# Kernel tuning notes

Measured on AMD Instinct MI355X. Metric: run time of the kernel, lower is better.

## Reference

```python
import jax, jax.numpy as jnp
import numpy as np

BS, T, D_IN = 128, 32, 128
DH = 128          # controller hidden size == memory word width M
N_SLOTS = 512     # memory rows
EPS = 1e-8


def _split_read(o):
    # o: [bs, M+6] -> k, beta, g, s(3), gamma
    k = o[:, :DH]
    beta = jax.nn.softplus(o[:, DH])
    g = jax.nn.sigmoid(o[:, DH + 1])
    s = jax.nn.softmax(o[:, DH + 2:DH + 5], axis=-1)
    gamma = 1.0 + jax.nn.softplus(o[:, DH + 5])
    return k, beta, g, s, gamma


def _attention(k, beta, g, s, gamma, mem, w_prev):
    # content addressing: cosine similarity sharpened by beta
    dot = jnp.einsum('bnm,bm->bn', mem, k)
    denom = jnp.linalg.norm(mem, axis=-1) * jnp.linalg.norm(k, axis=-1, keepdims=True) + EPS
    w_c = jax.nn.softmax(beta[:, None] * dot / denom, axis=-1)
    # gate interpolation with previous weights
    w_g = g[:, None] * w_c + (1.0 - g[:, None]) * w_prev
    # circular shift convolution over offsets {-1, 0, +1}
    w_t = (s[:, 0:1] * jnp.roll(w_g, -1, axis=-1)
           + s[:, 1:2] * w_g
           + s[:, 2:3] * jnp.roll(w_g, 1, axis=-1))
    # sharpening
    w = w_t ** gamma[:, None]
    return w / (jnp.sum(w, axis=-1, keepdims=True) + EPS)


def setup_inputs() -> dict:
    key = jax.random.key(0)
    ks = jax.random.split(key, 8)
    sc = lambda fan_in: 1.0 / np.sqrt(fan_in)
    return {
        'x':    jax.random.normal(ks[0], (BS, T, D_IN), jnp.float32),
        'Wxh':  jax.random.normal(ks[1], (D_IN, DH), jnp.float32) * sc(D_IN),
        'Whh':  jax.random.normal(ks[2], (DH, DH), jnp.float32) * sc(DH),
        'Wrh':  jax.random.normal(ks[3], (DH, DH), jnp.float32) * sc(DH),
        'bh':   jnp.zeros((DH,), jnp.float32),
        'Wout': jax.random.normal(ks[4], (DH + DH, D_IN), jnp.float32) * sc(2 * DH),
        'bout': jnp.zeros((D_IN,), jnp.float32),
        'Wr':   jax.random.normal(ks[5], (DH, DH + 6), jnp.float32) * sc(DH),
        'br':   jnp.zeros((DH + 6,), jnp.float32),
        'Ww':   jax.random.normal(ks[6], (DH, 3 * DH + 6), jnp.float32) * sc(DH),
        'bw':   jnp.zeros((3 * DH + 6,), jnp.float32),
    }


def reference(x, Wxh, Whh, Wrh, bh, Wout, bout, Wr, br, Ww, bw):
    bs = x.shape[0]
    h0 = jnp.zeros((bs, DH), x.dtype)
    r0 = jnp.zeros((bs, DH), x.dtype)
    w0 = jnp.full((bs, N_SLOTS), 1.0 / N_SLOTS, x.dtype)
    mem0 = jnp.full((bs, N_SLOTS, DH), 1e-6, x.dtype)

    def step(carry, x_t):
        h, r, w_prev, mem = carry
        # controller state
        h = jnp.tanh(x_t @ Wxh + h @ Whh + r @ Wrh + bh)
        # head parameter projections
        o_r = h @ Wr + br
        o_w = h @ Ww + bw
        k_r, b_r, g_r, s_r, y_r = _split_read(o_r)
        k_w, b_w_, g_w, s_w, y_w = _split_read(o_w[:, :DH + 6])
        e = jax.nn.sigmoid(o_w[:, DH + 6:2 * DH + 6])   # erase [bs, M]
        a = jnp.tanh(o_w[:, 2 * DH + 6:3 * DH + 6])     # add   [bs, M]
        # addressing (w_previous updated sequentially, read then write)
        w_r = _attention(k_r, b_r, g_r, s_r, y_r, mem, w_prev)
        w_w = _attention(k_w, b_w_, g_w, s_w, y_w, mem, w_r)
        # read
        r = jnp.einsum('bn,bnm->bm', w_r, mem)
        # erase / add write
        mem = mem * (1.0 - w_w[:, :, None] * e[:, None, :]) + w_w[:, :, None] * a[:, None, :]
        # output
        y = jnp.concatenate([h, r], axis=-1) @ Wout + bout
        return (h, r, w_w, mem), y

    _, ys = jax.lax.scan(step, (h0, r0, w0, mem0), jnp.swapaxes(x, 0, 1))
    return jnp.swapaxes(ys, 0, 1)  # [bs, ft, d_output]
```

## Files before the change

### kernel.cpp

```cpp
#include <hip/hip_runtime.h>
#include <hip/hip_bf16.h>
#include <math.h>

#define NT 1024
#define BSZ 128
#define TSTEPS 32
#define DIN 128
#define DHH 128
#define NSLOT 512
#define EPSF 1e-8f

static constexpr int F_FLOATS = 7160;
static constexpr size_t LDS_BYTES = 131072 + F_FLOATS * sizeof(float);

__device__ __forceinline__ float bf_lo(unsigned u) {
  union { unsigned u; float f; } c; c.u = u << 16; return c.f;
}
__device__ __forceinline__ float bf_hi(unsigned u) {
  union { unsigned u; float f; } c; c.u = u & 0xffff0000u; return c.f;
}
__device__ __forceinline__ unsigned short f2us(float f) {
  union { unsigned short s; __hip_bfloat16 h; } c; c.h = __float2bfloat16(f); return c.s;
}
__device__ __forceinline__ unsigned pkbf(float a, float b) {
  union { __hip_bfloat162 h2; unsigned u; } c;
  c.h2 = __float22bfloat162_rn(make_float2(a, b));
  return c.u;
}
__device__ __forceinline__ float sigmoid_(float x) { return 1.0f / (1.0f + __expf(-x)); }
__device__ __forceinline__ float softplus_(float x) {
  return fmaxf(x, 0.0f) + log1pf(__expf(-fabsf(x)));
}
__device__ __forceinline__ float tanh_(float x) {
  float e = __expf(-2.0f * fabsf(x));
  float t = (1.0f - e) / (1.0f + e);
  return copysignf(t, x);
}
__device__ __forceinline__ float waveSum(float v) {
#pragma unroll
  for (int m = 32; m >= 1; m >>= 1) v += __shfl_xor(v, m);
  return v;
}

__device__ __forceinline__ void bar_lds() {
  asm volatile("s_waitcnt lgkmcnt(0)" ::: "memory");
  __builtin_amdgcn_s_barrier();
}

__global__ __launch_bounds__(NT, 4)
void ntm_kernel(const float* __restrict__ x,
                const float* __restrict__ Wxh,
                const float* __restrict__ Whh,
                const float* __restrict__ Wrh,
                const float* __restrict__ bh,
                const float* __restrict__ Wout,
                const float* __restrict__ bout,
                const float* __restrict__ Wr,
                const float* __restrict__ br,
                const float* __restrict__ Ww,
                const float* __restrict__ bw,
                float* __restrict__ out)
{
  extern __shared__ char smem[];
  uint4* memv = (uint4*)smem;
  float* F = (float*)(smem + 131072);

  const int b = blockIdx.x;
  const int tid = threadIdx.x;
  const int g = tid >> 4, l = tid & 15;
  const int lane = tid & 63, wid = tid >> 6;

  float* U      = F + 0;
  float* yP     = F + 2560;
  float* sWprev = F + 4608;
  float* sP1    = F + 5632;
  float* sOr    = F + 6144;
  float* sOw    = F + 6288;
  float* sXt    = F + 6680;
  float* sH     = F + 6808;
  float* sR     = F + 6936;
  float* sP     = F + 7064;
  float* V      = sXt;
  uint4* krP    = (uint4*)(sP1 + 0);
  uint4* kwP    = (uint4*)(sP1 + 64);
  float* eR     = U + 0;
  float* eW     = U + 512;
  float2* sWW2  = (float2*)(U + 1024);

  {
    const unsigned short mb = f2us(1e-6f);
    const unsigned w32 = ((unsigned)mb << 16) | mb;
    const uint4 fv = make_uint4(w32, w32, w32, w32);
    for (int i = tid; i < NSLOT * DHH / 8; i += NT) memv[i] = fv;
  }
  for (int i = tid; i < NSLOT; i += NT) sWprev[i] = 1.0f / NSLOT;
  if (tid < DHH) { sH[tid] = 0.0f; sR[tid] = 0.0f; }
  if (tid < DIN) sXt[tid] = x[(size_t)b * TSTEPS * DIN + tid];
  __syncthreads();

  for (int t = 0; t < TSTEPS; ++t) {
    {
      const int q = tid & 63, s = tid >> 6;
      const int j2 = q * 2, i0 = s * 24;
      float2 acc = make_float2(0.f, 0.f);
#pragma unroll 2
      for (int k = 0; k < 6; ++k) {
        const float4 vv = *(const float4*)(V + i0 + 4 * k);
        const float vk[4] = { vv.x, vv.y, vv.z, vv.w };
#pragma unroll
        for (int u = 0; u < 4; ++u) {
          const int i = i0 + 4 * k + u;
          const float* Wp = (i < 128) ? (Wxh + i * DHH)
                          : (i < 256) ? (Whh + (i - 128) * DHH)
                                      : (Wrh + (i - 256) * DHH);
          const float2 wv = *(const float2*)(Wp + j2);
          acc.x = fmaf(vk[u], wv.x, acc.x);
          acc.y = fmaf(vk[u], wv.y, acc.y);
        }
      }
      *(float2*)(U + s * 128 + j2) = acc;
      if (t > 0 && tid < 512) {
        const int j4 = (tid & 31) * 4, sl = tid >> 5;
        float4 acc4 = *(const float4*)(yP + sl * 128 + j4);
#pragma unroll
        for (int w = 0; w < 8; ++w) {
          const float v = sR[8 * sl + w];
          const float4 wv = *(const float4*)(Wout + (128 + 8 * sl + w) * DIN + j4);
          acc4.x = fmaf(v, wv.x, acc4.x); acc4.y = fmaf(v, wv.y, acc4.y);
          acc4.z = fmaf(v, wv.z, acc4.z); acc4.w = fmaf(v, wv.w, acc4.w);
        }
        *(float4*)(yP + sl * 128 + j4) = acc4;
      }
      bar_lds();
    }
    if (tid < DHH) {
      float a2 = bh[tid];
#pragma unroll
      for (int q2 = 0; q2 < 16; ++q2) a2 += U[q2 * 128 + tid];
      sH[tid] = tanh_(a2);
    }
    bar_lds();

    {
      {
        const int s = tid;
        const int q = (s >= 786) ? 3 : (s >= 524) ? 2 : (s >= 262) ? 1 : 0;
        const int P = s - 262 * q;
        const int i0 = 32 * q;
        const float2* p;
        int strideF2;
        if (P < 67) { p = (const float2*)(Wr + i0 * 134 + 2 * P); strideF2 = 67; }
        else        { p = (const float2*)(Ww + i0 * 390 + 2 * (P - 67)); strideF2 = 195; }
        float2 acc = make_float2(0.f, 0.f);
#pragma unroll 2
        for (int k = 0; k < 8; ++k) {
          const float4 hv = *(const float4*)(sH + i0 + 4 * k);
          const float hk[4] = { hv.x, hv.y, hv.z, hv.w };
#pragma unroll
          for (int u = 0; u < 4; ++u) {
            const float2 wv = p[(4 * k + u) * strideF2];
            acc.x = fmaf(hk[u], wv.x, acc.x);
            acc.y = fmaf(hk[u], wv.y, acc.y);
          }
        }
        *(float2*)(U + s * 2) = acc;
      }
      if (lane < 3) {
        const int hs = wid * 3 + lane;
        const int e = hs >> 1, hh = hs & 1;
        const int cp = 171 + e;
        const int i0 = 96 + 16 * hh;
        const float2* p = (const float2*)(Ww + i0 * 390 + 2 * cp);
        float2 acc = make_float2(0.f, 0.f);
#pragma unroll 8
        for (int w = 0; w < 16; ++w) {
          const float v = sH[i0 + w];
          const float2 wv = *p;
          acc.x = fmaf(v, wv.x, acc.x);
          acc.y = fmaf(v, wv.y, acc.y);
          p += 195;
        }
        U[2096 + hs * 2]     = acc.x;
        U[2096 + hs * 2 + 1] = acc.y;
      }
      if (tid == 1023) {
        sP[0] = 0.f; sP[1] = 0.f; sP[2] = 0.f; sP[3] = 0.f; sP[4] = 0.f; sP[5] = 0.f;
      }
      bar_lds();
    }

    {
      if (tid < 134) {
        float v = 0.f;
#pragma unroll
        for (int q = 0; q < 4; ++q) v += U[tid + 524 * q];
        v += br[tid];
        sOr[tid] = v;
        if (tid < 128) {
          float s2 = waveSum(v * v);
          if (lane == 0) atomicAdd(&sP[0], s2);
        }
      } else if (tid == 134) {
        float sc[6];
#pragma unroll
        for (int j = 0; j < 6; ++j) {
          float v = 0.f;
#pragma unroll
          for (int q = 0; q < 4; ++q) v += U[(128 + j) + 524 * q];
          sc[j] = v + br[128 + j];
        }
        sP[80] = softplus_(sc[0]);
        sP[81] = sigmoid_(sc[1]);
        float mx = fmaxf(sc[2], fmaxf(sc[3], sc[4]));
        float e0 = __expf(sc[2] - mx), e1 = __expf(sc[3] - mx), e2 = __expf(sc[4] - mx);
        float es = e0 + e1 + e2;
        sP[82] = e0 / es; sP[83] = e1 / es; sP[84] = e2 / es;
        sP[85] = 1.0f + softplus_(sc[5]);
      } else if (tid == 135) {
        float sc[6];
#pragma unroll
        for (int j = 0; j < 6; ++j) {
          float v = 0.f;
#pragma unroll
          for (int q = 0; q < 4; ++q) v += U[(262 + j) + 524 * q];
          sc[j] = v + bw[128 + j];
        }
        sP[86] = softplus_(sc[0]);
        sP[87] = sigmoid_(sc[1]);
        float mx = fmaxf(sc[2], fmaxf(sc[3], sc[4]));
        float e0 = __expf(sc[2] - mx), e1 = __expf(sc[3] - mx), e2 = __expf(sc[4] - mx);
        float es = e0 + e1 + e2;
        sP[88] = e0 / es; sP[89] = e1 / es; sP[90] = e2 / es;
        sP[91] = 1.0f + softplus_(sc[5]);
      } else if (tid >= 256 && tid < 512) {
        const int cc = tid + 12;
        float v = U[cc] + U[cc + 524] + U[cc + 1048];
        if (cc < 476) {
          v += U[cc + 1572];
        } else {
          const int cw = cc - 134;
          const int e = (cw >> 1) - 171;
          const int base = 2096 + 4 * e + (cw & 1);
          v += U[base] + U[base + 2];
        }
        v += bw[tid - 122];
        sOw[tid - 120] = (tid < 384) ? sigmoid_(v) : tanh_(v);
      } else if (tid >= 512 && tid < 640) {
        const int cw = tid - 512;
        float v = 0.f;
#pragma unroll
        for (int q = 0; q < 4; ++q) v += U[(134 + cw) + 524 * q];
        v += bw[cw];
        sOw[cw] = v;
        float s2 = waveSum(v * v);
        if (lane == 0) atomicAdd(&sP[1], s2);
      } else if (tid >= 640 && tid < 768) {
        sR[tid - 640] = 0.f;
      } else if (tid >= 768 && tid < 800) {
        const int t2 = tid - 768;
        const int c = t2 & 15;
        union { uint4 v; unsigned short h[8]; } pk;
#pragma unroll
        for (int j = 0; j < 8; ++j) {
          const int col = c * 8 + j;
          float v = 0.f;
#pragma unroll
          for (int q = 0; q < 4; ++q)
            v += U[((t2 < 16) ? col : (134 + col)) + 524 * q];
          v += (t2 < 16) ? br[col] : bw[col];
          pk.h[j] = f2us(v);
        }
        if (t2 < 16) krP[c] = pk.v; else kwP[c] = pk.v;
      } else if (tid >= 896) {
        if (t > 0) {
          const int c = tid - 896;
          float y = bout[c];
#pragma unroll
          for (int q = 0; q < 16; ++q) y += yP[q * 128 + c];
          out[((size_t)b * TSTEPS + (t - 1)) * DIN + c] = y;
        }
      }
      bar_lds();
    }

    {
      const float kn_r = sqrtf(sP[0]);
      const float kn_w = sqrtf(sP[1]);
      const float beta_r = sP[80], beta_w = sP[86];
      const int n = tid >> 1, hf = tid & 1;
      const int sw = (n >> 2) & 3;
      float dr = 0.f, dw = 0.f, ss = 0.f;
#pragma unroll
      for (int c = 0; c < 8; ++c) {
        const int cl = hf * 8 + c;
        const uint4 mv = memv[n * 16 + (cl ^ sw)];
        const uint4 kr = krP[cl];
        const uint4 kw = kwP[cl];
        const unsigned mw_[4] = { mv.x, mv.y, mv.z, mv.w };
        const unsigned krw[4] = { kr.x, kr.y, kr.z, kr.w };
        const unsigned kww[4] = { kw.x, kw.y, kw.z, kw.w };
#pragma unroll
        for (int j = 0; j < 4; ++j) {
          const float m0 = bf_lo(mw_[j]), m1 = bf_hi(mw_[j]);
          dr = fmaf(m0, bf_lo(krw[j]), dr); dr = fmaf(m1, bf_hi(krw[j]), dr);
          dw = fmaf(m0, bf_lo(kww[j]), dw); dw = fmaf(m1, bf_hi(kww[j]), dw);
          ss = fmaf(m0, m0, ss);            ss = fmaf(m1, m1, ss);
        }
      }
      dr += __shfl_xor(dr, 1);
      dw += __shfl_xor(dw, 1);
      ss += __shfl_xor(ss, 1);
      const float nr = sqrtf(ss);
      const float er = __expf(beta_r * dr / (nr * kn_r + EPSF));
      const float ew = __expf(beta_w * dw / (nr * kn_w + EPSF));
      if (hf == 0) { eR[n] = er; eW[n] = ew; }
      float s1 = waveSum(er) * 0.5f;
      float s2 = waveSum(ew) * 0.5f;
      if (lane == 0) { atomicAdd(&sP[2], s1); atomicAdd(&sP[3], s2); }
      bar_lds();
    }

    {
      if (tid < NSLOT) {
        const float invE = 1.0f / sP[2];
        const float gr = sP[81], omg = 1.0f - sP[81];
        const int im = (tid - 1) & 511, ip = (tid + 1) & 511;
        const float wgm = gr * (eR[im] * invE) + omg * sWprev[im];
        const float wg0 = gr * (eR[tid] * invE) + omg * sWprev[tid];
        const float wgp = gr * (eR[ip] * invE) + omg * sWprev[ip];
        const float wt = sP[82] * wgp + sP[83] * wg0 + sP[84] * wgm;
        float p1 = (wt > 0.0f) ? __expf(sP[85] * __logf(wt)) : 0.0f;
        float P = waveSum(p1);
        sP1[tid] = p1;
        if (lane == 0) atomicAdd(&sP[4], P);
      } else {
        const int p = tid - 512;
        const int j4 = (p & 31) * 4, sl = p >> 5;
        float4 acc = make_float4(0.f, 0.f, 0.f, 0.f);
#pragma unroll
        for (int w = 0; w < 8; ++w) {
          const float v = sH[8 * sl + w];
          const float4 wv = *(const float4*)(Wout + (8 * sl + w) * DIN + j4);
          acc.x = fmaf(v, wv.x, acc.x); acc.y = fmaf(v, wv.y, acc.y);
          acc.z = fmaf(v, wv.z, acc.z); acc.w = fmaf(v, wv.w, acc.w);
        }
        *(float4*)(yP + sl * 128 + j4) = acc;
      }
      bar_lds();
    }
    {
      if (tid < NSLOT) {
        const float pinv1 = 1.0f / (sP[4] + EPSF);
        const float invE = 1.0f / sP[3];
        const float gw = sP[87], omg = 1.0f - sP[87];
        const int im = (tid - 1) & 511, ip = (tid + 1) & 511;
        const float wgm = gw * (eW[im] * invE) + omg * (sP1[im] * pinv1);
        const float wg0 = gw * (eW[tid] * invE) + omg * (sP1[tid] * pinv1);
        const float wgp = gw * (eW[ip] * invE) + omg * (sP1[ip] * pinv1);
        const float wt = sP[88] * wgp + sP[89] * wg0 + sP[90] * wgm;
        float p2 = (wt > 0.0f) ? __expf(sP[91] * __logf(wt)) : 0.0f;
        float P = waveSum(p2);
        sWW2[tid] = make_float2(sP1[tid] * pinv1, p2);
        if (lane == 0) atomicAdd(&sP[5], P);
      } else if (tid < 512 + DIN && t + 1 < TSTEPS) {
        const int i = tid - 512;
        sXt[i] = x[((size_t)b * TSTEPS + (t + 1)) * DIN + i];
      }
      bar_lds();
    }

    {
      const float pinv2 = 1.0f / (sP[5] + EPSF);
      if (tid < NSLOT) sWprev[tid] = sWW2[tid].y * pinv2;

      const int cl = l ^ ((g >> 2) & 3);
      float4 e4a = *(const float4*)(sOw + 136 + cl * 8);
      float4 e4b = *(const float4*)(sOw + 140 + cl * 8);
      float4 a4a = *(const float4*)(sOw + 264 + cl * 8);
      float4 a4b = *(const float4*)(sOw + 268 + cl * 8);
      const float e8[8] = { e4a.x, e4a.y, e4a.z, e4a.w, e4b.x, e4b.y, e4b.z, e4b.w };
      const float a8[8] = { a4a.x, a4a.y, a4a.z, a4a.w, a4b.x, a4b.y, a4b.z, a4b.w };
      float r8[8] = { 0, 0, 0, 0, 0, 0, 0, 0 };
#pragma unroll 2
      for (int it = 0; it < 8; ++it) {
        const int n = g + 64 * it;
        const float2 wn = sWW2[n];
        const float wrn = wn.x;
        const float wwn = wn.y * pinv2;
        uint4 pk = memv[n * 16 + l];
        const unsigned wds[4] = { pk.x, pk.y, pk.z, pk.w };
        float m[8];
#pragma unroll
        for (int j = 0; j < 4; ++j) { m[2 * j] = bf_lo(wds[j]); m[2 * j + 1] = bf_hi(wds[j]); }
#pragma unroll
        for (int j = 0; j < 8; ++j) {
          r8[j] = fmaf(wrn, m[j], r8[j]);
          const float d = fmaf(-e8[j], m[j], a8[j]);
          m[j] = fmaf(wwn, d, m[j]);
        }
        pk.x = pkbf(m[0], m[1]);
        pk.y = pkbf(m[2], m[3]);
        pk.z = pkbf(m[4], m[5]);
        pk.w = pkbf(m[6], m[7]);
        memv[n * 16 + l] = pk;
      }
#pragma unroll
      for (int j = 0; j < 8; ++j) {
        r8[j] += __shfl_xor(r8[j], 16);
        r8[j] += __shfl_xor(r8[j], 32);
      }
      if (lane < 16) {
#pragma unroll
        for (int j = 0; j < 8; ++j) atomicAdd(&sR[cl * 8 + j], r8[j]);
      }
      bar_lds();
    }
  }

  if (tid < 512) {
    const int j4 = (tid & 31) * 4, sl = tid >> 5;
    float4 acc = *(const float4*)(yP + sl * 128 + j4);
#pragma unroll
    for (int w = 0; w < 8; ++w) {
      const float v = sR[8 * sl + w];
      const float4 wv = *(const float4*)(Wout + (128 + 8 * sl + w) * DIN + j4);
      acc.x = fmaf(v, wv.x, acc.x); acc.y = fmaf(v, wv.y, acc.y);
      acc.z = fmaf(v, wv.z, acc.z); acc.w = fmaf(v, wv.w, acc.w);
    }
    *(float4*)(yP + sl * 128 + j4) = acc;
  }
  bar_lds();
  if (tid < DIN) {
    float y = bout[tid];
#pragma unroll
    for (int q = 0; q < 16; ++q) y += yP[q * 128 + tid];
    out[((size_t)b * TSTEPS + (TSTEPS - 1)) * DIN + tid] = y;
  }
}

extern "C" void kernel_launch(void* const* d_in, const int* in_sizes, int n_in,
                              void* d_out, int out_size, void* d_ws, size_t ws_size,
                              hipStream_t stream) {
  (void)in_sizes; (void)n_in; (void)out_size; (void)d_ws; (void)ws_size;
  hipFuncSetAttribute(reinterpret_cast<const void*>(ntm_kernel),
                      hipFuncAttributeMaxDynamicSharedMemorySize, (int)LDS_BYTES);
  ntm_kernel<<<dim3(BSZ), dim3(NT), LDS_BYTES, stream>>>(
      (const float*)d_in[0], (const float*)d_in[1], (const float*)d_in[2],
      (const float*)d_in[3], (const float*)d_in[4], (const float*)d_in[5],
      (const float*)d_in[6], (const float*)d_in[7], (const float*)d_in[8],
      (const float*)d_in[9], (const float*)d_in[10],
      (float*)d_out);
}
```

Baseline: 841.8 us.

## Precompute next step's x@Wxh and h@Whh during idle attention phase

```diff
diff --git a/kernel.cpp b/kernel.cpp
--- a/kernel.cpp
+++ b/kernel.cpp
@@ -73,6 +73,7 @@
   float* U      = F + 0;
   float* yP     = F + 2560;
   float* sWprev = F + 4608;
+  float* xhP    = F + 5120;
   float* sP1    = F + 5632;
   float* sOr    = F + 6144;
   float* sOw    = F + 6288;
@@ -80,7 +81,6 @@
   float* sH     = F + 6808;
   float* sR     = F + 6936;
   float* sP     = F + 7064;
-  float* V      = sXt;
   uint4* krP    = (uint4*)(sP1 + 0);
   uint4* kwP    = (uint4*)(sP1 + 64);
   float* eR     = U + 0;
@@ -98,25 +98,32 @@
   if (tid < DIN) sXt[tid] = x[(size_t)b * TSTEPS * DIN + tid];
   __syncthreads();
 
+  if (tid >= 512) {
+    const int p = tid - 512;
+    const int c = p & 127, q4 = p >> 7;
+    const float* Wp; const float* vsrc;
+    if (q4 < 2) { Wp = Wxh + (q4 * 64) * DHH + c; vsrc = sXt + q4 * 64; }
+    else        { Wp = Whh + ((q4 - 2) * 64) * DHH + c; vsrc = sH + (q4 - 2) * 64; }
+    float acc = 0.f;
+#pragma unroll 8
+    for (int w = 0; w < 64; ++w) acc = fmaf(vsrc[w], Wp[w * DHH], acc);
+    xhP[q4 * 128 + c] = acc;
+  }
+  __syncthreads();
+
   for (int t = 0; t < TSTEPS; ++t) {
     {
       const int q = tid & 63, s = tid >> 6;
-      const int j2 = q * 2, i0 = s * 24;
+      const int j2 = q * 2, i0 = s * 8;
+      const float4 ra = *(const float4*)(sR + i0);
+      const float4 rb = *(const float4*)(sR + i0 + 4);
+      const float rv[8] = { ra.x, ra.y, ra.z, ra.w, rb.x, rb.y, rb.z, rb.w };
       float2 acc = make_float2(0.f, 0.f);
-#pragma unroll 2
-      for (int k = 0; k < 6; ++k) {
-        const float4 vv = *(const float4*)(V + i0 + 4 * k);
-        const float vk[4] = { vv.x, vv.y, vv.z, vv.w };
-#pragma unroll
-        for (int u = 0; u < 4; ++u) {
-          const int i = i0 + 4 * k + u;
-          const float* Wp = (i < 128) ? (Wxh + i * DHH)
-                          : (i < 256) ? (Whh + (i - 128) * DHH)
-                                      : (Wrh + (i - 256) * DHH);
-          const float2 wv = *(const float2*)(Wp + j2);
-          acc.x = fmaf(vk[u], wv.x, acc.x);
-          acc.y = fmaf(vk[u], wv.y, acc.y);
-        }
+#pragma unroll
+      for (int u = 0; u < 8; ++u) {
+        const float2 wv = *(const float2*)(Wrh + (i0 + u) * DHH + j2);
+        acc.x = fmaf(rv[u], wv.x, acc.x);
+        acc.y = fmaf(rv[u], wv.y, acc.y);
       }
       *(float2*)(U + s * 128 + j2) = acc;
       if (t > 0 && tid < 512) {
@@ -137,6 +144,8 @@
       float a2 = bh[tid];
 #pragma unroll
       for (int q2 = 0; q2 < 16; ++q2) a2 += U[q2 * 128 + tid];
+#pragma unroll
+      for (int q2 = 0; q2 < 4; ++q2) a2 += xhP[q2 * 128 + tid];
       sH[tid] = tanh_(a2);
     }
     bar_lds();
@@ -232,7 +241,12 @@
         float es = e0 + e1 + e2;
         sP[88] = e0 / es; sP[89] = e1 / es; sP[90] = e2 / es;
         sP[91] = 1.0f + softplus_(sc[5]);
-      } else if (tid >= 256 && tid < 512) {
+      } else if (tid < 256) {
+        if (t + 1 < TSTEPS) {
+          const int i = tid - 136;
+          sXt[i] = x[((size_t)b * TSTEPS + (t + 1)) * DIN + i];
+        }
+      } else if (tid < 512) {
         const int cc = tid + 12;
         float v = U[cc] + U[cc + 524] + U[cc + 1048];
         if (cc < 476) {
@@ -245,7 +259,7 @@
         }
         v += bw[tid - 122];
         sOw[tid - 120] = (tid < 384) ? sigmoid_(v) : tanh_(v);
-      } else if (tid >= 512 && tid < 640) {
+      } else if (tid < 640) {
         const int cw = tid - 512;
         float v = 0.f;
 #pragma unroll
@@ -254,9 +268,9 @@
         sOw[cw] = v;
         float s2 = waveSum(v * v);
         if (lane == 0) atomicAdd(&sP[1], s2);
-      } else if (tid >= 640 && tid < 768) {
+      } else if (tid < 768) {
         sR[tid - 640] = 0.f;
-      } else if (tid >= 768 && tid < 800) {
+      } else if (tid < 800) {
         const int t2 = tid - 768;
         const int c = t2 & 15;
         union { uint4 v; unsigned short h[8]; } pk;
@@ -271,6 +285,11 @@
           pk.h[j] = f2us(v);
         }
         if (t2 < 16) krP[c] = pk.v; else kwP[c] = pk.v;
+      } else if (tid < 808) {
+        if (t + 1 < TSTEPS) {
+          const int i = 120 + (tid - 800);
+          sXt[i] = x[((size_t)b * TSTEPS + (t + 1)) * DIN + i];
+        }
       } else if (tid >= 896) {
         if (t > 0) {
           const int c = tid - 896;
@@ -362,9 +381,16 @@
         float P = waveSum(p2);
         sWW2[tid] = make_float2(sP1[tid] * pinv1, p2);
         if (lane == 0) atomicAdd(&sP[5], P);
-      } else if (tid < 512 + DIN && t + 1 < TSTEPS) {
-        const int i = tid - 512;
-        sXt[i] = x[((size_t)b * TSTEPS + (t + 1)) * DIN + i];
+      } else if (t + 1 < TSTEPS) {
+        const int p = tid - 512;
+        const int c = p & 127, q4 = p >> 7;
+        const float* Wp; const float* vsrc;
+        if (q4 < 2) { Wp = Wxh + (q4 * 64) * DHH + c; vsrc = sXt + q4 * 64; }
+        else        { Wp = Whh + ((q4 - 2) * 64) * DHH + c; vsrc = sH + (q4 - 2) * 64; }
+        float acc = 0.f;
+#pragma unroll 8
+        for (int w = 0; w < 64; ++w) acc = fmaf(vsrc[w], Wp[w * DHH], acc);
+        xhP[q4 * 128 + c] = acc;
       }
       bar_lds();
     }
```

Result: slower. 940.8 us (+11.8%).
